# Performance work log

Measured on AMD Instinct MI355X. Metric: run time of the kernel, lower is better.

The kernel has to match this reference:

```python
import jax, jax.numpy as jnp
import numpy as np

N, E = 50000, 800000
NODE_DIM, EDGE_DIM = 96, 64
IN_DIM = 2 * NODE_DIM + EDGE_DIM  # 256


def setup_inputs() -> dict:
    key = jax.random.key(0)
    k = jax.random.split(key, 7)
    h = jax.random.normal(k[0], (N, NODE_DIM), dtype=jnp.float32)
    edge_index = jax.random.randint(k[1], (2, E), 0, N, dtype=jnp.int64)
    edge_attr = jax.random.normal(k[2], (E, EDGE_DIM), dtype=jnp.float32)
    # Linear params (PyTorch default-ish scale)
    s = 1.0 / np.sqrt(IN_DIM)
    W_e = jax.random.uniform(k[3], (IN_DIM, NODE_DIM), jnp.float32, -s, s)
    b_e = jax.random.uniform(k[4], (NODE_DIM,), jnp.float32, -s, s)
    W_n = jax.random.uniform(k[5], (IN_DIM, NODE_DIM), jnp.float32, -s, s)
    b_n = jax.random.uniform(k[6], (NODE_DIM,), jnp.float32, -s, s)
    return {"h": h, "edge_index": edge_index, "edge_attr": edge_attr,
            "W_e": W_e, "b_e": b_e, "W_n": W_n, "b_n": b_n}


def reference(h, edge_index, edge_attr, W_e, b_e, W_n, b_n):
    src, dst = edge_index[0], edge_index[1]
    concat = jnp.concatenate([h[src], h[dst], edge_attr], axis=-1)  # [E, 256]
    gates = jax.nn.sigmoid(concat @ W_e + b_e)                      # [E, node_dim]
    messages = jax.nn.softplus(concat @ W_n + b_n)                  # [E, node_dim]
    gated = gates * messages
    n = h.shape[0]
    h_new = jax.ops.segment_sum(gated, dst, num_segments=n)         # [N, node_dim]
    edge_count = jax.ops.segment_sum(jnp.ones((dst.shape[0],), h.dtype), dst, num_segments=n)
    edge_count = jnp.clip(edge_count, 1.0, None)[:, None]
    return h + h_new / edge_count
```

## Files before the change

### kernel.cpp

```cpp
#include <hip/hip_runtime.h>
#include <hip/hip_bf16.h>


#define NODE_DIM 96
#define EDGE_DIM 64
#define IN_DIM   256
#define NT_TILES 12
#define KT_TILES 8

typedef float  f32x4  __attribute__((ext_vector_type(4)));
typedef __bf16 bf16x8 __attribute__((ext_vector_type(8)));

__device__ __forceinline__ unsigned short bf16rne(float f) {
    unsigned int u = __float_as_uint(f);
    u += 0x7FFFu + ((u >> 16) & 1u);
    return (unsigned short)(u >> 16);
}

__global__ void pack_w_kernel(const float* __restrict__ We,
                              const float* __restrict__ Wn,
                              unsigned short* __restrict__ bpack) {
    int t = blockIdx.x * blockDim.x + threadIdx.x;
    if (t >= KT_TILES * NT_TILES * 64) return;
    int tile = t >> 6, lane = t & 63;
    int kt = tile / NT_TILES, nt = tile % NT_TILES;
    const float* W = (nt < 6) ? We : Wn;
    int n  = (nt % 6) * 16 + (lane & 15);
    int k0 = kt * 32 + (lane >> 4) * 8;
    union { unsigned short u[8]; uint4 v; } tmp;
#pragma unroll
    for (int j = 0; j < 8; ++j) tmp.u[j] = bf16rne(W[(k0 + j) * NODE_DIM + n]);
    *(uint4*)(bpack + (size_t)t * 8) = tmp.v;
}

__global__ void cvt_h_kernel(const float* __restrict__ h,
                             unsigned short* __restrict__ hb, int total8) {
    int i = blockIdx.x * 256 + threadIdx.x;
    if (i >= total8) return;
    const float4 v0 = ((const float4*)h)[i * 2];
    const float4 v1 = ((const float4*)h)[i * 2 + 1];
    union { unsigned short u[8]; uint4 v; } p;
    p.u[0] = bf16rne(v0.x); p.u[1] = bf16rne(v0.y);
    p.u[2] = bf16rne(v0.z); p.u[3] = bf16rne(v0.w);
    p.u[4] = bf16rne(v1.x); p.u[5] = bf16rne(v1.y);
    p.u[6] = bf16rne(v1.z); p.u[7] = bf16rne(v1.w);
    ((uint4*)hb)[i] = p.v;
}

__global__ void hist_kernel(const int* __restrict__ eidx, unsigned* __restrict__ deg, int E) {
    int e = blockIdx.x * 256 + threadIdx.x;
    if (e < E) atomicAdd(deg + eidx[E + e], 1u);
}

__device__ __forceinline__ unsigned block_excl_scan_256(unsigned v, int tid,
                                                        unsigned* wsum, unsigned* wpre,
                                                        unsigned* total) {
    int lane = tid & 63, w = tid >> 6;
    unsigned inc = v;
#pragma unroll
    for (int o = 1; o < 64; o <<= 1) {
        unsigned t = __shfl_up(inc, o, 64);
        if (lane >= o) inc += t;
    }
    if (lane == 63) wsum[w] = inc;
    __syncthreads();
    if (tid == 0) {
        unsigned s = 0;
#pragma unroll
        for (int k = 0; k < 4; ++k) { wpre[k] = s; s += wsum[k]; }
        *total = s;
    }
    __syncthreads();
    return inc - v + wpre[w];
}

__global__ void scan_block_kernel(const unsigned* __restrict__ deg,
                                  unsigned* __restrict__ scanned,
                                  unsigned* __restrict__ blocksum, int N) {
    __shared__ unsigned wsum[4], wpre[4], total;
    int tid = threadIdx.x;
    int i = blockIdx.x * 256 + tid;
    unsigned v = (i < N) ? deg[i] : 0u;
    unsigned excl = block_excl_scan_256(v, tid, wsum, wpre, &total);
    if (i < N) scanned[i] = excl;
    if (tid == 0) blocksum[blockIdx.x] = total;
}

__global__ void scan_sums_kernel(const unsigned* __restrict__ blocksum,
                                 unsigned* __restrict__ blockpref, int NB) {
    __shared__ unsigned wsum[4], wpre[4], total;
    int tid = threadIdx.x;
    unsigned v = (tid < NB) ? blocksum[tid] : 0u;
    unsigned excl = block_excl_scan_256(v, tid, wsum, wpre, &total);
    if (tid < NB) blockpref[tid] = excl;
}

__global__ void scan_finalize_kernel(const unsigned* __restrict__ scanned,
                                     const unsigned* __restrict__ blockpref,
                                     unsigned* __restrict__ offsets,
                                     unsigned* __restrict__ cursor, int N, int E) {
    int i = blockIdx.x * 256 + threadIdx.x;
    if (i < N) {
        unsigned o = scanned[i] + blockpref[i >> 8];
        offsets[i] = o;
        cursor[i]  = o;
    }
    if (i == 0) offsets[N] = (unsigned)E;
}

__global__ void scatter_kernel(const int* __restrict__ eidx,
                               unsigned* __restrict__ cursor,
                               unsigned* __restrict__ rank, int E) {
    int e = blockIdx.x * 256 + threadIdx.x;
    if (e < E) {
        int d = eidx[E + e];
        rank[e] = atomicAdd(cursor + d, 1u);
    }
}

__global__ __launch_bounds__(256, 3)
void gemm_msg_kernel(const unsigned short* __restrict__ hb,
                     const int*   __restrict__ eidx,
                     const float* __restrict__ ea,
                     const unsigned short* __restrict__ bpack,
                     const float* __restrict__ be,
                     const float* __restrict__ bn,
                     const unsigned* __restrict__ rank,
                     unsigned short* __restrict__ msg,
                     int E) {
    const int tid  = threadIdx.x;
    const int wave = tid >> 6, lane = tid & 63;
    const int m    = lane & 15;
    const int quad = lane >> 4;
    const int base = blockIdx.x * 128 + wave * 32;

    const unsigned short* hsq[2];
    const unsigned short* hdq[2];
    const float*          epq[2];
#pragma unroll
    for (int mt = 0; mt < 2; ++mt) {
        int e  = base + mt * 16 + m;
        int eg = (e < E) ? e : (E - 1);
        int src = eidx[eg];
        int dst = eidx[E + eg];
        hsq[mt] = hb + (size_t)src * NODE_DIM + quad * 8;
        hdq[mt] = hb + (size_t)dst * NODE_DIM + quad * 8;
        epq[mt] = ea + (size_t)eg  * EDGE_DIM + quad * 8;
    }
    const unsigned short* bl = bpack + lane * 8;

    f32x4 acc[2][NT_TILES];
#pragma unroll
    for (int mt = 0; mt < 2; ++mt)
#pragma unroll
        for (int nt = 0; nt < NT_TILES; ++nt) acc[mt][nt] = (f32x4){0.f, 0.f, 0.f, 0.f};

#pragma unroll
    for (int kt = 0; kt < KT_TILES; ++kt) {
        bf16x8 A[2];
#pragma unroll
        for (int mt = 0; mt < 2; ++mt) {
            if (kt < 3) {
                A[mt] = *(const bf16x8*)(hsq[mt] + kt * 32);
            } else if (kt < 6) {
                A[mt] = *(const bf16x8*)(hdq[mt] + (kt - 3) * 32);
            } else {
                const float4 v0 = *(const float4*)(epq[mt] + (kt - 6) * 32);
                const float4 v1 = *(const float4*)(epq[mt] + (kt - 6) * 32 + 4);
                union { unsigned short u[8]; bf16x8 b; } t;
                t.u[0] = bf16rne(v0.x); t.u[1] = bf16rne(v0.y);
                t.u[2] = bf16rne(v0.z); t.u[3] = bf16rne(v0.w);
                t.u[4] = bf16rne(v1.x); t.u[5] = bf16rne(v1.y);
                t.u[6] = bf16rne(v1.z); t.u[7] = bf16rne(v1.w);
                A[mt] = t.b;
            }
        }
#pragma unroll
        for (int nt = 0; nt < NT_TILES; ++nt) {
            bf16x8 bfrag = *(const bf16x8*)(bl + (kt * NT_TILES + nt) * 512);
            acc[0][nt] = __builtin_amdgcn_mfma_f32_16x16x32_bf16(A[0], bfrag, acc[0][nt], 0, 0, 0);
            acc[1][nt] = __builtin_amdgcn_mfma_f32_16x16x32_bf16(A[1], bfrag, acc[1][nt], 0, 0, 0);
        }
    }

#pragma unroll
    for (int mt = 0; mt < 2; ++mt) {
#pragma unroll
        for (int r = 0; r < 4; ++r) {
            const int ee = base + mt * 16 + quad * 4 + r;
            if (ee >= E) continue;
            const size_t prow = (size_t)rank[ee] * NODE_DIM;
#pragma unroll
            for (int nt = 0; nt < 6; ++nt) {
                const int col = nt * 16 + m;
                float g  = acc[mt][nt][r]     + be[col];
                float mm = acc[mt][nt + 6][r] + bn[col];
                float gate = 1.0f / (1.0f + __expf(-g));
                float sp   = fmaxf(mm, 0.0f) + __logf(1.0f + __expf(-fabsf(mm)));
                msg[prow + col] = bf16rne(gate * sp);
            }
        }
    }
}

__global__ __launch_bounds__(256)
void aggregate_kernel(const float* __restrict__ h,
                      const unsigned* __restrict__ offsets,
                      const unsigned short* __restrict__ msg,
                      float* __restrict__ out, int N) {
    int t = blockIdx.x * 256 + threadIdx.x;
    int n = t / 12, g = t % 12;
    if (n >= N) return;

    const unsigned o0 = offsets[n];
    const unsigned o1 = offsets[n + 1];
    const int deg = (int)(o1 - o0);

    float s0 = 0.f, s1 = 0.f, s2 = 0.f, s3 = 0.f;
    float s4 = 0.f, s5 = 0.f, s6 = 0.f, s7 = 0.f;
    for (unsigned k = o0; k < o1; ++k) {
        const uint4 v = *(const uint4*)(msg + (size_t)k * NODE_DIM + g * 8);
        s0 += __uint_as_float((v.x & 0xFFFFu) << 16);
        s1 += __uint_as_float(v.x & 0xFFFF0000u);
        s2 += __uint_as_float((v.y & 0xFFFFu) << 16);
        s3 += __uint_as_float(v.y & 0xFFFF0000u);
        s4 += __uint_as_float((v.z & 0xFFFFu) << 16);
        s5 += __uint_as_float(v.z & 0xFFFF0000u);
        s6 += __uint_as_float((v.w & 0xFFFFu) << 16);
        s7 += __uint_as_float(v.w & 0xFFFF0000u);
    }
    const float inv = 1.0f / (float)((deg > 0) ? deg : 1);
    const size_t basei = (size_t)n * NODE_DIM + g * 8;
    const float4 h0 = *(const float4*)(h + basei);
    const float4 h1 = *(const float4*)(h + basei + 4);
    float4 o0v = {h0.x + s0 * inv, h0.y + s1 * inv, h0.z + s2 * inv, h0.w + s3 * inv};
    float4 o1v = {h1.x + s4 * inv, h1.y + s5 * inv, h1.z + s6 * inv, h1.w + s7 * inv};
    *(float4*)(out + basei)     = o0v;
    *(float4*)(out + basei + 4) = o1v;
}

#define TILE_E 64
__global__ __launch_bounds__(256, 4)
void cgconv_atomic_kernel(const float* __restrict__ h,
                          const int*   __restrict__ eidx,
                          const float* __restrict__ ea,
                          const unsigned short* __restrict__ bpack,
                          const float* __restrict__ be,
                          const float* __restrict__ bn,
                          float* __restrict__ hnew,
                          float* __restrict__ cnt,
                          int E) {
    const int tid  = threadIdx.x;
    const int wave = tid >> 6, lane = tid & 63;
    const int m    = lane & 15;
    const int quad = lane >> 4;

    const int e  = blockIdx.x * TILE_E + wave * 16 + m;
    const int eg = (e < E) ? e : (E - 1);
    const int src = eidx[eg];
    const int dst = eidx[E + eg];
    if (quad == 0 && e < E) unsafeAtomicAdd(cnt + dst, 1.0f);

    f32x4 acc[NT_TILES];
#pragma unroll
    for (int nt = 0; nt < NT_TILES; ++nt) acc[nt] = (f32x4){0.f, 0.f, 0.f, 0.f};

    const float* hsrc = h + (size_t)src * NODE_DIM;
    const float* hdst = h + (size_t)dst * NODE_DIM;
    const float* earo = ea + (size_t)eg * EDGE_DIM;

#pragma unroll
    for (int kt = 0; kt < KT_TILES; ++kt) {
        const int ko = kt * 32 + quad * 8;
        const float* p;
        if (kt < 3)      p = hsrc + ko;
        else if (kt < 6) p = hdst + (ko - NODE_DIM);
        else             p = earo + (ko - 2 * NODE_DIM);
        const float4 v0 = *(const float4*)p;
        const float4 v1 = *(const float4*)(p + 4);
        union { unsigned short u[8]; bf16x8 b; } A;
        A.u[0] = bf16rne(v0.x); A.u[1] = bf16rne(v0.y);
        A.u[2] = bf16rne(v0.z); A.u[3] = bf16rne(v0.w);
        A.u[4] = bf16rne(v1.x); A.u[5] = bf16rne(v1.y);
        A.u[6] = bf16rne(v1.z); A.u[7] = bf16rne(v1.w);
#pragma unroll
        for (int nt = 0; nt < NT_TILES; ++nt) {
            bf16x8 bfrag = *(const bf16x8*)(bpack +
                             (size_t)((kt * NT_TILES + nt) * 64 + lane) * 8);
            acc[nt] = __builtin_amdgcn_mfma_f32_16x16x32_bf16(A.b, bfrag, acc[nt], 0, 0, 0);
        }
    }

    int drow[4], erow[4];
#pragma unroll
    for (int r = 0; r < 4; ++r) {
        drow[r] = __shfl(dst, quad * 4 + r, 64);
        erow[r] = blockIdx.x * TILE_E + wave * 16 + quad * 4 + r;
    }
#pragma unroll
    for (int nt = 0; nt < 6; ++nt) {
        const int col = nt * 16 + m;
        const float bev = be[col];
        const float bnv = bn[col];
#pragma unroll
        for (int r = 0; r < 4; ++r) {
            if (erow[r] >= E) continue;
            float g  = acc[nt][r] + bev;
            float mm = acc[nt + 6][r] + bnv;
            float gate = 1.0f / (1.0f + __expf(-g));
            float sp   = fmaxf(mm, 0.0f) + __logf(1.0f + __expf(-fabsf(mm)));
            unsafeAtomicAdd(hnew + (size_t)drow[r] * NODE_DIM + col, gate * sp);
        }
    }
}

__global__ void finalize_kernel(const float* __restrict__ h,
                                const float* __restrict__ hnew,
                                const float* __restrict__ cnt,
                                float* __restrict__ out,
                                int total4) {
    int i = blockIdx.x * blockDim.x + threadIdx.x;
    if (i >= total4) return;
    int n = i / 24;
    float inv = 1.0f / fmaxf(cnt[n], 1.0f);
    float4 hv = ((const float4*)h)[i];
    float4 av = ((const float4*)hnew)[i];
    float4 o = {hv.x + av.x * inv, hv.y + av.y * inv, hv.z + av.z * inv, hv.w + av.w * inv};
    ((float4*)out)[i] = o;
}

extern "C" void kernel_launch(void* const* d_in, const int* in_sizes, int n_in,
                              void* d_out, int out_size, void* d_ws, size_t ws_size,
                              hipStream_t stream) {
    const float* h   = (const float*)d_in[0];
    const int*   ei  = (const int*)  d_in[1];
    const float* ea  = (const float*)d_in[2];
    const float* We  = (const float*)d_in[3];
    const float* be  = (const float*)d_in[4];
    const float* Wn  = (const float*)d_in[5];
    const float* bn  = (const float*)d_in[6];

    const int N = in_sizes[0] / NODE_DIM;
    const int E = in_sizes[2] / EDGE_DIM;
    char* ws = (char*)d_ws;

    size_t off = 0;
    auto take = [&](size_t bytes) { size_t o = off; off = (off + bytes + 511) & ~(size_t)511; return o; };
    const size_t O_BPACK  = take((size_t)KT_TILES * NT_TILES * 64 * 16);
    const size_t O_DEG    = take((size_t)N * 4);
    const size_t O_SCAN   = take((size_t)N * 4);
    const size_t O_BSUM   = take(1024);
    const size_t O_BPREF  = take(1024);
    const size_t O_OFFS   = take((size_t)(N + 1) * 4);
    const size_t O_CURS   = take((size_t)N * 4);
    const size_t O_RANK   = take((size_t)E * 4);
    const size_t O_HB     = take((size_t)N * NODE_DIM * 2);
    const size_t O_MSG    = take((size_t)E * NODE_DIM * 2);
    const size_t NEED = off;

    unsigned short* bpack = (unsigned short*)(ws + O_BPACK);
    pack_w_kernel<<<(KT_TILES * NT_TILES * 64 + 255) / 256, 256, 0, stream>>>(We, Wn, bpack);

    if (ws_size >= NEED) {
        unsigned* deg    = (unsigned*)(ws + O_DEG);
        unsigned* scn    = (unsigned*)(ws + O_SCAN);
        unsigned* bsum   = (unsigned*)(ws + O_BSUM);
        unsigned* bpref  = (unsigned*)(ws + O_BPREF);
        unsigned* offs   = (unsigned*)(ws + O_OFFS);
        unsigned* curs   = (unsigned*)(ws + O_CURS);
        unsigned* rank   = (unsigned*)(ws + O_RANK);
        unsigned short* hb  = (unsigned short*)(ws + O_HB);
        unsigned short* msg = (unsigned short*)(ws + O_MSG);

        hipMemsetAsync(deg, 0, (size_t)N * 4, stream);

        const int total8 = N * NODE_DIM / 8;
        cvt_h_kernel<<<(total8 + 255) / 256, 256, 0, stream>>>(h, hb, total8);

        const int NB = (N + 255) / 256;
        hist_kernel<<<(E + 255) / 256, 256, 0, stream>>>(ei, deg, E);
        scan_block_kernel<<<NB, 256, 0, stream>>>(deg, scn, bsum, N);
        scan_sums_kernel<<<1, 256, 0, stream>>>(bsum, bpref, NB);
        scan_finalize_kernel<<<NB, 256, 0, stream>>>(scn, bpref, offs, curs, N, E);
        scatter_kernel<<<(E + 255) / 256, 256, 0, stream>>>(ei, curs, rank, E);

        gemm_msg_kernel<<<(E + 127) / 128, 256, 0, stream>>>(hb, ei, ea, bpack, be, bn, rank, msg, E);

        const int aggthreads = N * 12;
        aggregate_kernel<<<(aggthreads + 255) / 256, 256, 0, stream>>>(h, offs, msg, (float*)d_out, N);
    } else {
        size_t cnt_off  = O_DEG;
        size_t hnew_off = (cnt_off + (size_t)N * 4 + 511) & ~(size_t)511;
        float* cnt  = (float*)(ws + cnt_off);
        float* hnew = (float*)(ws + hnew_off);
        hipMemsetAsync(ws + cnt_off, 0, hnew_off - cnt_off + (size_t)N * NODE_DIM * 4, stream);
        cgconv_atomic_kernel<<<(E + TILE_E - 1) / TILE_E, 256, 0, stream>>>(
            h, ei, ea, bpack, be, bn, hnew, cnt, E);
        const int total4 = N * (NODE_DIM / 4);
        finalize_kernel<<<(total4 + 255) / 256, 256, 0, stream>>>(h, hnew, cnt, (float*)d_out, total4);
    }
}
```

Baseline: 634.4 us.

## Make gemm kernel persistent with register-resident weight fragments

The message GEMM becomes a persistent grid of 1024 single-wave blocks. Each wave loads the full packed weight matrix (96 bf16x8 fragments) and the biases into registers once, then loops over 16-edge tiles with a grid stride. This removes the repeated per-tile reloads of B and bias from global/L2. The cost is heavy VGPR pressure that limits occupancy, fewer waves to hide gather latency, and only one M tile per wave, so each B fragment is reused less per load.

```diff
diff --git a/kernel.cpp b/kernel.cpp
--- a/kernel.cpp
+++ b/kernel.cpp
@@ -7,6 +7,8 @@
 #define IN_DIM   256
 #define NT_TILES 12
 #define KT_TILES 8
+
+#define GEMM_GRID 1024
 
 typedef float  f32x4  __attribute__((ext_vector_type(4)));
 typedef __bf16 bf16x8 __attribute__((ext_vector_type(8)));
@@ -118,7 +120,7 @@
     }
 }
 
-__global__ __launch_bounds__(256, 3)
+__global__ __launch_bounds__(64, 1)
 void gemm_msg_kernel(const unsigned short* __restrict__ hb,
                      const int*   __restrict__ eidx,
                      const float* __restrict__ ea,
@@ -128,73 +130,73 @@
                      const unsigned* __restrict__ rank,
                      unsigned short* __restrict__ msg,
                      int E) {
-    const int tid  = threadIdx.x;
-    const int wave = tid >> 6, lane = tid & 63;
+    const int lane = threadIdx.x;
     const int m    = lane & 15;
     const int quad = lane >> 4;
-    const int base = blockIdx.x * 128 + wave * 32;
-
-    const unsigned short* hsq[2];
-    const unsigned short* hdq[2];
-    const float*          epq[2];
-#pragma unroll
-    for (int mt = 0; mt < 2; ++mt) {
-        int e  = base + mt * 16 + m;
-        int eg = (e < E) ? e : (E - 1);
-        int src = eidx[eg];
-        int dst = eidx[E + eg];
-        hsq[mt] = hb + (size_t)src * NODE_DIM + quad * 8;
-        hdq[mt] = hb + (size_t)dst * NODE_DIM + quad * 8;
-        epq[mt] = ea + (size_t)eg  * EDGE_DIM + quad * 8;
-    }
-    const unsigned short* bl = bpack + lane * 8;
-
-    f32x4 acc[2][NT_TILES];
-#pragma unroll
-    for (int mt = 0; mt < 2; ++mt)
-#pragma unroll
-        for (int nt = 0; nt < NT_TILES; ++nt) acc[mt][nt] = (f32x4){0.f, 0.f, 0.f, 0.f};
-
-#pragma unroll
-    for (int kt = 0; kt < KT_TILES; ++kt) {
-        bf16x8 A[2];
-#pragma unroll
-        for (int mt = 0; mt < 2; ++mt) {
+
+    bf16x8 B[KT_TILES][NT_TILES];
+    {
+        const bf16x8* bp = (const bf16x8*)bpack + lane;
+#pragma unroll
+        for (int kt = 0; kt < KT_TILES; ++kt)
+#pragma unroll
+            for (int nt = 0; nt < NT_TILES; ++nt)
+                B[kt][nt] = bp[(kt * NT_TILES + nt) * 64];
+    }
+
+    float bev[6], bnv[6];
+#pragma unroll
+    for (int nt = 0; nt < 6; ++nt) {
+        bev[nt] = be[nt * 16 + m];
+        bnv[nt] = bn[nt * 16 + m];
+    }
+
+    const int STRIDE = GEMM_GRID * 16;
+    for (int base = blockIdx.x * 16; base < E; base += STRIDE) {
+        const int e  = base + m;
+        const int eg = (e < E) ? e : (E - 1);
+        const int src = eidx[eg];
+        const int dst = eidx[E + eg];
+        const unsigned short* hs = hb + (size_t)src * NODE_DIM + quad * 8;
+        const unsigned short* hd = hb + (size_t)dst * NODE_DIM + quad * 8;
+        const float*          ep = ea + (size_t)eg  * EDGE_DIM + quad * 8;
+
+        f32x4 acc[NT_TILES];
+#pragma unroll
+        for (int nt = 0; nt < NT_TILES; ++nt) acc[nt] = (f32x4){0.f, 0.f, 0.f, 0.f};
+
+#pragma unroll
+        for (int kt = 0; kt < KT_TILES; ++kt) {
+            bf16x8 A;
             if (kt < 3) {
-                A[mt] = *(const bf16x8*)(hsq[mt] + kt * 32);
+                A = *(const bf16x8*)(hs + kt * 32);
             } else if (kt < 6) {
-                A[mt] = *(const bf16x8*)(hdq[mt] + (kt - 3) * 32);
+                A = *(const bf16x8*)(hd + (kt - 3) * 32);
             } else {
-                const float4 v0 = *(const float4*)(epq[mt] + (kt - 6) * 32);
-                const float4 v1 = *(const float4*)(epq[mt] + (kt - 6) * 32 + 4);
+                const float4 v0 = *(const float4*)(ep + (kt - 6) * 32);
+                const float4 v1 = *(const float4*)(ep + (kt - 6) * 32 + 4);
                 union { unsigned short u[8]; bf16x8 b; } t;
                 t.u[0] = bf16rne(v0.x); t.u[1] = bf16rne(v0.y);
                 t.u[2] = bf16rne(v0.z); t.u[3] = bf16rne(v0.w);
                 t.u[4] = bf16rne(v1.x); t.u[5] = bf16rne(v1.y);
                 t.u[6] = bf16rne(v1.z); t.u[7] = bf16rne(v1.w);
-                A[mt] = t.b;
+                A = t.b;
             }
+#pragma unroll
+            for (int nt = 0; nt < NT_TILES; ++nt)
+                acc[nt] = __builtin_amdgcn_mfma_f32_16x16x32_bf16(A, B[kt][nt], acc[nt], 0, 0, 0);
         }
-#pragma unroll
-        for (int nt = 0; nt < NT_TILES; ++nt) {
-            bf16x8 bfrag = *(const bf16x8*)(bl + (kt * NT_TILES + nt) * 512);
-            acc[0][nt] = __builtin_amdgcn_mfma_f32_16x16x32_bf16(A[0], bfrag, acc[0][nt], 0, 0, 0);
-            acc[1][nt] = __builtin_amdgcn_mfma_f32_16x16x32_bf16(A[1], bfrag, acc[1][nt], 0, 0, 0);
-        }
-    }
-
-#pragma unroll
-    for (int mt = 0; mt < 2; ++mt) {
+
 #pragma unroll
         for (int r = 0; r < 4; ++r) {
-            const int ee = base + mt * 16 + quad * 4 + r;
+            const int ee = base + quad * 4 + r;
             if (ee >= E) continue;
             const size_t prow = (size_t)rank[ee] * NODE_DIM;
 #pragma unroll
             for (int nt = 0; nt < 6; ++nt) {
                 const int col = nt * 16 + m;
-                float g  = acc[mt][nt][r]     + be[col];
-                float mm = acc[mt][nt + 6][r] + bn[col];
+                float g  = acc[nt][r]     + bev[nt];
+                float mm = acc[nt + 6][r] + bnv[nt];
                 float gate = 1.0f / (1.0f + __expf(-g));
                 float sp   = fmaxf(mm, 0.0f) + __logf(1.0f + __expf(-fabsf(mm)));
                 msg[prow + col] = bf16rne(gate * sp);
@@ -384,7 +386,7 @@
         scan_finalize_kernel<<<NB, 256, 0, stream>>>(scn, bpref, offs, curs, N, E);
         scatter_kernel<<<(E + 255) / 256, 256, 0, stream>>>(ei, curs, rank, E);
 
-        gemm_msg_kernel<<<(E + 127) / 128, 256, 0, stream>>>(hb, ei, ea, bpack, be, bn, rank, msg, E);
+        gemm_msg_kernel<<<GEMM_GRID, 64, 0, stream>>>(hb, ei, ea, bpack, be, bn, rank, msg, E);
 
         const int aggthreads = N * 12;
         aggregate_kernel<<<(aggthreads + 255) / 256, 256, 0, stream>>>(h, offs, msg, (float*)d_out, N);
```

New measurement: 707.1 us. 1.11x slower.

## Persistent GEMM kernel with register-resident weights split across waves by output column

Applied to the files above, without the earlier changes.

Turns the edge GEMM into a persistent kernel with a fixed grid that loops over 32-edge tiles. Each of six waves keeps its own gate and message weight columns in registers for the whole kernel instead of reloading them per tile. Edge indices for the next tile are prefetched, and rank lookups are hoisted ahead of the epilogue. The cost is that all six waves reload the same A rows (gathered h and edge_attr) for every tile, so A-side gather traffic rises while B reloads and accumulator register pressure fall.

```diff
diff --git a/kernel.cpp b/kernel.cpp
--- a/kernel.cpp
+++ b/kernel.cpp
@@ -7,6 +7,10 @@
 #define IN_DIM   256
 #define NT_TILES 12
 #define KT_TILES 8
+
+#define GEMM_GRID   2048
+#define GEMM_WAVES  6
+#define GEMM_THREADS (GEMM_WAVES * 64)
 
 typedef float  f32x4  __attribute__((ext_vector_type(4)));
 typedef __bf16 bf16x8 __attribute__((ext_vector_type(8)));
@@ -118,7 +122,7 @@
     }
 }
 
-__global__ __launch_bounds__(256, 3)
+__global__ __launch_bounds__(GEMM_THREADS, 3)
 void gemm_msg_kernel(const unsigned short* __restrict__ hb,
                      const int*   __restrict__ eidx,
                      const float* __restrict__ ea,
@@ -132,74 +136,114 @@
     const int wave = tid >> 6, lane = tid & 63;
     const int m    = lane & 15;
     const int quad = lane >> 4;
-    const int base = blockIdx.x * 128 + wave * 32;
-
-    const unsigned short* hsq[2];
-    const unsigned short* hdq[2];
-    const float*          epq[2];
+
+    bf16x8 Bg[KT_TILES], Bm[KT_TILES];
+    {
+        const bf16x8* bp = (const bf16x8*)bpack + lane;
+#pragma unroll
+        for (int kt = 0; kt < KT_TILES; ++kt) {
+            Bg[kt] = bp[(kt * NT_TILES + wave) * 64];
+            Bm[kt] = bp[(kt * NT_TILES + wave + 6) * 64];
+        }
+    }
+    const int   col = wave * 16 + m;
+    const float bev = be[col];
+    const float bnv = bn[col];
+
+    int csrc[2], cdst[2], nsrc[2], ndst[2];
 #pragma unroll
     for (int mt = 0; mt < 2; ++mt) {
-        int e  = base + mt * 16 + m;
+        int e  = blockIdx.x * 32 + mt * 16 + m;
         int eg = (e < E) ? e : (E - 1);
-        int src = eidx[eg];
-        int dst = eidx[E + eg];
-        hsq[mt] = hb + (size_t)src * NODE_DIM + quad * 8;
-        hdq[mt] = hb + (size_t)dst * NODE_DIM + quad * 8;
-        epq[mt] = ea + (size_t)eg  * EDGE_DIM + quad * 8;
-    }
-    const unsigned short* bl = bpack + lane * 8;
-
-    f32x4 acc[2][NT_TILES];
-#pragma unroll
-    for (int mt = 0; mt < 2; ++mt)
-#pragma unroll
-        for (int nt = 0; nt < NT_TILES; ++nt) acc[mt][nt] = (f32x4){0.f, 0.f, 0.f, 0.f};
-
-#pragma unroll
-    for (int kt = 0; kt < KT_TILES; ++kt) {
-        bf16x8 A[2];
+        csrc[mt] = eidx[eg];
+        cdst[mt] = eidx[E + eg];
+    }
+
+    for (int t = blockIdx.x; (long)t * 32 < E; t += GEMM_GRID) {
+        const int base = t * 32;
+
+        const unsigned short* hsq[2];
+        const unsigned short* hdq[2];
+        const float*          epq[2];
 #pragma unroll
         for (int mt = 0; mt < 2; ++mt) {
-            if (kt < 3) {
-                A[mt] = *(const bf16x8*)(hsq[mt] + kt * 32);
-            } else if (kt < 6) {
-                A[mt] = *(const bf16x8*)(hdq[mt] + (kt - 3) * 32);
-            } else {
-                const float4 v0 = *(const float4*)(epq[mt] + (kt - 6) * 32);
-                const float4 v1 = *(const float4*)(epq[mt] + (kt - 6) * 32 + 4);
-                union { unsigned short u[8]; bf16x8 b; } t;
-                t.u[0] = bf16rne(v0.x); t.u[1] = bf16rne(v0.y);
-                t.u[2] = bf16rne(v0.z); t.u[3] = bf16rne(v0.w);
-                t.u[4] = bf16rne(v1.x); t.u[5] = bf16rne(v1.y);
-                t.u[6] = bf16rne(v1.z); t.u[7] = bf16rne(v1.w);
-                A[mt] = t.b;
+            int e  = base + mt * 16 + m;
+            int eg = (e < E) ? e : (E - 1);
+            hsq[mt] = hb + (size_t)csrc[mt] * NODE_DIM + quad * 8;
+            hdq[mt] = hb + (size_t)cdst[mt] * NODE_DIM + quad * 8;
+            epq[mt] = ea + (size_t)eg  * EDGE_DIM + quad * 8;
+        }
+
+        unsigned prow_[2][4];
+#pragma unroll
+        for (int mt = 0; mt < 2; ++mt)
+#pragma unroll
+            for (int r = 0; r < 4; ++r) {
+                int ee = base + mt * 16 + quad * 4 + r;
+                prow_[mt][r] = rank[(ee < E) ? ee : (E - 1)];
             }
-        }
-#pragma unroll
-        for (int nt = 0; nt < NT_TILES; ++nt) {
-            bf16x8 bfrag = *(const bf16x8*)(bl + (kt * NT_TILES + nt) * 512);
-            acc[0][nt] = __builtin_amdgcn_mfma_f32_16x16x32_bf16(A[0], bfrag, acc[0][nt], 0, 0, 0);
-            acc[1][nt] = __builtin_amdgcn_mfma_f32_16x16x32_bf16(A[1], bfrag, acc[1][nt], 0, 0, 0);
-        }
-    }
-
-#pragma unroll
-    for (int mt = 0; mt < 2; ++mt) {
-#pragma unroll
-        for (int r = 0; r < 4; ++r) {
-            const int ee = base + mt * 16 + quad * 4 + r;
-            if (ee >= E) continue;
-            const size_t prow = (size_t)rank[ee] * NODE_DIM;
-#pragma unroll
-            for (int nt = 0; nt < 6; ++nt) {
-                const int col = nt * 16 + m;
-                float g  = acc[mt][nt][r]     + be[col];
-                float mm = acc[mt][nt + 6][r] + bn[col];
+
+        const int tn = t + GEMM_GRID;
+        if ((long)tn * 32 < E) {
+#pragma unroll
+            for (int mt = 0; mt < 2; ++mt) {
+                int e  = tn * 32 + mt * 16 + m;
+                int eg = (e < E) ? e : (E - 1);
+                nsrc[mt] = eidx[eg];
+                ndst[mt] = eidx[E + eg];
+            }
+        }
+
+        f32x4 accg[2], accm[2];
+#pragma unroll
+        for (int mt = 0; mt < 2; ++mt) {
+            accg[mt] = (f32x4){0.f, 0.f, 0.f, 0.f};
+            accm[mt] = (f32x4){0.f, 0.f, 0.f, 0.f};
+        }
+
+#pragma unroll
+        for (int kt = 0; kt < KT_TILES; ++kt) {
+            bf16x8 A[2];
+#pragma unroll
+            for (int mt = 0; mt < 2; ++mt) {
+                if (kt < 3) {
+                    A[mt] = *(const bf16x8*)(hsq[mt] + kt * 32);
+                } else if (kt < 6) {
+                    A[mt] = *(const bf16x8*)(hdq[mt] + (kt - 3) * 32);
+                } else {
+                    const float4 v0 = *(const float4*)(epq[mt] + (kt - 6) * 32);
+                    const float4 v1 = *(const float4*)(epq[mt] + (kt - 6) * 32 + 4);
+                    union { unsigned short u[8]; bf16x8 b; } tt;
+                    tt.u[0] = bf16rne(v0.x); tt.u[1] = bf16rne(v0.y);
+                    tt.u[2] = bf16rne(v0.z); tt.u[3] = bf16rne(v0.w);
+                    tt.u[4] = bf16rne(v1.x); tt.u[5] = bf16rne(v1.y);
+                    tt.u[6] = bf16rne(v1.z); tt.u[7] = bf16rne(v1.w);
+                    A[mt] = tt.b;
+                }
+            }
+#pragma unroll
+            for (int mt = 0; mt < 2; ++mt) {
+                accg[mt] = __builtin_amdgcn_mfma_f32_16x16x32_bf16(A[mt], Bg[kt], accg[mt], 0, 0, 0);
+                accm[mt] = __builtin_amdgcn_mfma_f32_16x16x32_bf16(A[mt], Bm[kt], accm[mt], 0, 0, 0);
+            }
+        }
+
+#pragma unroll
+        for (int mt = 0; mt < 2; ++mt) {
+#pragma unroll
+            for (int r = 0; r < 4; ++r) {
+                const int ee = base + mt * 16 + quad * 4 + r;
+                if (ee >= E) continue;
+                float g  = accg[mt][r] + bev;
+                float mm = accm[mt][r] + bnv;
                 float gate = 1.0f / (1.0f + __expf(-g));
                 float sp   = fmaxf(mm, 0.0f) + __logf(1.0f + __expf(-fabsf(mm)));
-                msg[prow + col] = bf16rne(gate * sp);
+                msg[(size_t)prow_[mt][r] * NODE_DIM + col] = bf16rne(gate * sp);
             }
         }
+
+#pragma unroll
+        for (int mt = 0; mt < 2; ++mt) { csrc[mt] = nsrc[mt]; cdst[mt] = ndst[mt]; }
     }
 }
 
@@ -384,7 +428,7 @@
         scan_finalize_kernel<<<NB, 256, 0, stream>>>(scn, bpref, offs, curs, N, E);
         scatter_kernel<<<(E + 255) / 256, 256, 0, stream>>>(ei, curs, rank, E);
 
-        gemm_msg_kernel<<<(E + 127) / 128, 256, 0, stream>>>(hb, ei, ea, bpack, be, bn, rank, msg, E);
+        gemm_msg_kernel<<<GEMM_GRID, GEMM_THREADS, 0, stream>>>(hb, ei, ea, bpack, be, bn, rank, msg, E);
 
         const int aggthreads = N * 12;
         aggregate_kernel<<<(aggthreads + 255) / 256, 256, 0, stream>>>(h, offs, msg, (float*)d_out, N);
```

Result: slower. 844.6 us (+33.1%).
